# Optimization experiments

Hardware: AMD Instinct MI355X
Metric: run time of the kernel (lower is better)

The kernel has to match this reference:

```python
import jax, jax.numpy as jnp
import numpy as np

N, C_IN, C_OUT, K, S, P, H, W = 16, 64, 128, 3, 1, 1, 224, 224

def setup_inputs() -> dict:
    key = jax.random.key(0)
    kx, kw = jax.random.split(key)
    x = jax.random.normal(kx, (N, C_IN, H, W), dtype=jnp.float32)
    weight = jax.random.normal(kw, (C_OUT, C_IN, K, K), dtype=jnp.float32)
    bias = jnp.zeros((C_OUT,), dtype=jnp.float32)
    return {"x": x, "weight": weight, "bias": bias}

def reference(x, weight, bias):
    # im2col + matmul with stride 1 is exactly a standard conv2d with SAME-style padding P
    out = jax.lax.conv_general_dilated(
        x, weight,
        window_strides=(S, S),
        padding=((P, P), (P, P)),
        dimension_numbers=("NCHW", "OIHW", "NCHW"),
    )
    return out + bias[None, :, None, None]  # [N, C_OUT, H, W]
```

## Files before the change

### kernel.cpp

```cpp
#include <hip/hip_runtime.h>
#include <cstdint>
#include <cstddef>


typedef short bf16x8 __attribute__((ext_vector_type(8)));
typedef float f32x4 __attribute__((ext_vector_type(4)));

#define N_ 16
#define CI_ 64
#define CO_ 128
#define H_ 224
#define W_ 224
#define HW_ (H_ * W_)

#define WP_ 226
#define CBS_ 1808ULL
#define HPS_ 14464ULL
#define NS_ 3268864ULL

#define ROWBUF_SHORTS 7296
#define CONV3_LDS 145408

__device__ __forceinline__ unsigned short f2bf(float f) {
    unsigned u = __builtin_bit_cast(unsigned, f);
    u += 0x7FFFu + ((u >> 16) & 1u);
    return (unsigned short)(u >> 16);
}

__global__ void prep_weight(const float* __restrict__ w, unsigned short* __restrict__ wr) {
    int i = blockIdx.x * 256 + threadIdx.x;
    if (i >= 9 * CO_ * CI_) return;
    int ci = i & 63;
    int co = (i >> 6) & 127;
    int t  = i >> 13;
    wr[i] = f2bf(w[(co * CI_ + ci) * 9 + t]);
}

__global__ __launch_bounds__(256) void prep_x(const float* __restrict__ x,
                                              unsigned short* __restrict__ xp) {
    int b = blockIdx.x;
    int n = b / 226, hp = b - n * 226;
    int tid = threadIdx.x;
    unsigned short* row = xp + (size_t)n * NS_ + (size_t)hp * HPS_;
    if (hp == 0 || hp == 225) {
        #pragma unroll
        for (int k = 0; k < 8; ++k) {
            int i = k * 256 + tid;
            if (i < 1808) ((uint4*)row)[i] = make_uint4(0, 0, 0, 0);
        }
        return;
    }
    int h = hp - 1;
    const float* xb = x + (size_t)n * CI_ * HW_ + (size_t)h * W_;
    for (int k = 0; k < 7; ++k) {
        int item = k * 256 + tid;
        int w = item % 224;
        int cb = item / 224;
        unsigned r[4];
        #pragma unroll
        for (int c = 0; c < 4; ++c) {
            float lo = xb[(size_t)(cb * 8 + 2 * c) * HW_ + w];
            float hi = xb[(size_t)(cb * 8 + 2 * c + 1) * HW_ + w];
            r[c] = (unsigned)f2bf(lo) | ((unsigned)f2bf(hi) << 16);
        }
        *(uint4*)(row + (size_t)cb * CBS_ + (size_t)(w + 1) * 8) = make_uint4(r[0], r[1], r[2], r[3]);
    }
    if (tid < 16) {
        int cb = tid >> 1, wp = (tid & 1) * 225;
        *(uint4*)(row + (size_t)cb * CBS_ + (size_t)wp * 8) = make_uint4(0, 0, 0, 0);
    }
}

__global__ __launch_bounds__(512, 2) void conv3(
    const unsigned short* __restrict__ xp, const unsigned short* __restrict__ wr,
    const float* __restrict__ bias, float* __restrict__ out)
{
    extern __shared__ __align__(16) unsigned short ring[];
    float* bounce = (float*)ring + 6 * ROWBUF_SHORTS / 2;

    int bid = blockIdx.x;
    int swz = (bid & 7) * 32 + (bid >> 3);
    int n = swz >> 4;
    int rem = swz & 15;
    int wseg = rem & 1;
    int strip = rem >> 1;
    int ho0 = strip * 28;

    int tid = threadIdx.x, lane = tid & 63, wid = tid >> 6;
    int hr = wid & 1, mq = wid >> 1;
    int lrow = lane & 15, lk = lane >> 4;

    const unsigned short* xpn = xp + (size_t)n * NS_;

    auto stage_row = [&](int hp) {
        const unsigned short* srow = xpn + (size_t)hp * HPS_ + (size_t)(wseg * 112) * 8;
        unsigned short* dbase = ring + (size_t)(hp % 6) * ROWBUF_SHORTS;
        int idx = tid;
        {
            int cb = idx / 114, wp = idx - cb * 114;
            __builtin_amdgcn_global_load_lds(
                (const __attribute__((address_space(1))) void*)(srow + (size_t)cb * CBS_ + (size_t)wp * 8),
                (__attribute__((address_space(3))) void*)(dbase + (size_t)idx * 8), 16, 0, 0);
        }
        idx = 512 + tid;
        if (idx < 912) {
            int cb = idx / 114, wp = idx - cb * 114;
            __builtin_amdgcn_global_load_lds(
                (const __attribute__((address_space(1))) void*)(srow + (size_t)cb * CBS_ + (size_t)wp * 8),
                (__attribute__((address_space(3))) void*)(dbase + (size_t)idx * 8), 16, 0, 0);
        }
    };

    stage_row(ho0); stage_row(ho0 + 1); stage_row(ho0 + 2); stage_row(ho0 + 3);
    __syncthreads();

    #pragma unroll 1
    for (int i = 0; i < 14; ++i) {
        int ho = ho0 + 2 * i;

        if (i < 13) { stage_row(ho + 4); stage_row(ho + 5); }

        f32x4 acc[2][7];
        #pragma unroll
        for (int a = 0; a < 2; ++a)
            #pragma unroll
            for (int b2 = 0; b2 < 7; ++b2)
                #pragma unroll
                for (int k = 0; k < 4; ++k)
                    acc[a][b2][k] = 0.0f;

        #pragma unroll
        for (int ch = 0; ch < 2; ++ch) {
            #pragma unroll
            for (int t = 0; t < 9; ++t) {
                int kh = t / 3, kw = t - kh * 3;
                bf16x8 afr[2];
                #pragma unroll
                for (int mf = 0; mf < 2; ++mf) {
                    size_t ai = ((size_t)(t * 128 + mq * 32 + mf * 16 + lrow)) * 64
                              + (size_t)(ch * 32 + lk * 8);
                    afr[mf] = *(const bf16x8*)(wr + ai);
                }
                int slot = (ho + hr + kh) % 6;
                int rb = slot * ROWBUF_SHORTS + ((ch * 4 + lk) * 114) * 8;
                int wb = lrow + kw;
                #pragma unroll
                for (int nf = 0; nf < 7; ++nf) {
                    bf16x8 bfr = *(const bf16x8*)(ring + rb + (size_t)(wb + nf * 16) * 8);
                    acc[0][nf] = __builtin_amdgcn_mfma_f32_16x16x32_bf16(afr[0], bfr, acc[0][nf], 0, 0, 0);
                    acc[1][nf] = __builtin_amdgcn_mfma_f32_16x16x32_bf16(afr[1], bfr, acc[1][nf], 0, 0, 0);
                }
            }
        }

        float* lf = bounce + wid * 1808;
        int h = ho + hr;
        #pragma unroll
        for (int mf = 0; mf < 2; ++mf) {
            float bv[4];
            #pragma unroll
            for (int r = 0; r < 4; ++r)
                bv[r] = bias[mq * 32 + mf * 16 + lk * 4 + r];
            float* wbase = lf + lk * 452 + lrow;
            #pragma unroll
            for (int r = 0; r < 4; ++r)
                #pragma unroll
                for (int nf = 0; nf < 7; ++nf)
                    wbase[r * 112 + nf * 16] = acc[mf][nf][r] + bv[r];
            #pragma unroll
            for (int j = 0; j < 7; ++j) {
                int idx4 = j * 64 + lane;
                int col = idx4 / 28;
                int w4  = idx4 - col * 28;
                f32x4 v = *(const f32x4*)(lf + (col >> 2) * 452 + (col & 3) * 112 + w4 * 4);
                size_t ob = (((size_t)n * CO_ + mq * 32 + mf * 16 + col) * H_ + h) * W_
                          + wseg * 112 + w4 * 4;
                *(f32x4*)(out + ob) = v;
            }
        }

        __syncthreads();
    }
}

__global__ __launch_bounds__(256, 2) void conv2(
    const unsigned short* __restrict__ xp, const unsigned short* __restrict__ wr,
    const float* __restrict__ bias, float* __restrict__ out)
{
    __shared__ __align__(16) unsigned short xs[4 * 8 * 114 * 8];

    int bid = blockIdx.x;
    int swz = (bid & 7) * 448 + (bid >> 3);
    int n = swz / 224;
    int r2 = swz - n * 224;
    int hblk = r2 >> 1;
    int wseg = r2 & 1;
    int h0 = hblk * 2;

    int tid = threadIdx.x, lane = tid & 63, wid = tid >> 6;
    int hr = wid & 1, mh = wid >> 1;
    int lrow = lane & 15, lk = lane >> 4;

    f32x4 acc[4][7];
    #pragma unroll
    for (int a = 0; a < 4; ++a)
        #pragma unroll
        for (int b2 = 0; b2 < 7; ++b2)
            #pragma unroll
            for (int k = 0; k < 4; ++k)
                acc[a][b2][k] = 0.0f;

    const unsigned short* xpn = xp + (size_t)n * NS_;

    #pragma unroll
    for (int it = 0; it < 14; ++it) {
        int idx = it * 256 + tid;
        int wp = idx % 114;
        int rc = idx / 114;
        const unsigned short* src = xpn + (size_t)(h0 + (rc >> 3)) * HPS_
                                  + (size_t)(rc & 7) * CBS_ + (size_t)(wseg * 112 + wp) * 8;
        __builtin_amdgcn_global_load_lds(
            (const __attribute__((address_space(1))) void*)src,
            (__attribute__((address_space(3))) void*)(xs + (size_t)idx * 8), 16, 0, 0);
    }
    if (tid < 64) {
        int idx = 3584 + tid;
        int wp = idx % 114;
        int rc = idx / 114;
        const unsigned short* src = xpn + (size_t)(h0 + (rc >> 3)) * HPS_
                                  + (size_t)(rc & 7) * CBS_ + (size_t)(wseg * 112 + wp) * 8;
        __builtin_amdgcn_global_load_lds(
            (const __attribute__((address_space(1))) void*)src,
            (__attribute__((address_space(3))) void*)(xs + (size_t)idx * 8), 16, 0, 0);
    }
    __syncthreads();

    #pragma unroll
    for (int ch = 0; ch < 2; ++ch) {
        #pragma unroll
        for (int t = 0; t < 9; ++t) {
            int kh = t / 3, kw = t - kh * 3;
            bf16x8 afr[4];
            #pragma unroll
            for (int mf = 0; mf < 4; ++mf) {
                size_t ai = ((size_t)(t * 128 + mh * 64 + mf * 16 + lrow)) * 64
                          + (size_t)(ch * 32 + lk * 8);
                afr[mf] = *(const bf16x8*)(wr + ai);
            }
            int rbase = ((hr + kh) * 8 + ch * 4 + lk) * 114;
            int wpb = lrow + kw;
            #pragma unroll
            for (int nf = 0; nf < 7; ++nf) {
                bf16x8 bfr = *(const bf16x8*)(&xs[(size_t)(rbase + wpb + nf * 16) * 8]);
                #pragma unroll
                for (int mf = 0; mf < 4; ++mf)
                    acc[mf][nf] = __builtin_amdgcn_mfma_f32_16x16x32_bf16(
                        afr[mf], bfr, acc[mf][nf], 0, 0, 0);
            }
        }
    }

    __syncthreads();
    float* lf = (float*)xs;
    int h = h0 + hr;
    #pragma unroll
    for (int mf = 0; mf < 4; ++mf) {
        float bv[4];
        #pragma unroll
        for (int r = 0; r < 4; ++r)
            bv[r] = bias[mh * 64 + mf * 16 + lk * 4 + r];
        float* wbase = lf + wid * 1808 + lk * 452 + lrow;
        #pragma unroll
        for (int r = 0; r < 4; ++r)
            #pragma unroll
            for (int nf = 0; nf < 7; ++nf)
                wbase[r * 112 + nf * 16] = acc[mf][nf][r] + bv[r];
        #pragma unroll
        for (int j = 0; j < 7; ++j) {
            int idx4 = j * 64 + lane;
            int col = idx4 / 28;
            int w4  = idx4 - col * 28;
            f32x4 v = *(const f32x4*)(lf + wid * 1808 + (col >> 2) * 452 + (col & 3) * 112 + w4 * 4);
            size_t ob = (((size_t)n * CO_ + mh * 64 + mf * 16 + col) * H_ + h) * W_
                      + wseg * 112 + w4 * 4;
            *(f32x4*)(out + ob) = v;
        }
    }
}

__global__ __launch_bounds__(512, 2) void conv_mfma(
    const float* __restrict__ x, const unsigned short* __restrict__ wr,
    const float* __restrict__ bias, float* __restrict__ out)
{
    __shared__ unsigned short xs[4 * 4 * 226 * 8];
    int bid = blockIdx.x;
    int swz = (bid & 7) * 224 + (bid >> 3);
    int n = swz / 112;
    int hblk = swz - n * 112;
    int h0 = hblk * 2;
    int tid = threadIdx.x;
    int lane = tid & 63;
    int wid = tid >> 6;
    int hr = wid & 1, nh = (wid >> 1) & 1, mh = wid >> 2;
    int lrow = lane & 15, lk = lane >> 4;

    f32x4 acc[4][7];
    #pragma unroll
    for (int a = 0; a < 4; ++a)
        #pragma unroll
        for (int b = 0; b < 7; ++b)
            #pragma unroll
            for (int k = 0; k < 4; ++k)
                acc[a][b][k] = 0.0f;

    for (int ch = 0; ch < 2; ++ch) {
        if (ch) __syncthreads();
        const float* xb = x + ((size_t)n * CI_ + (size_t)ch * 32) * HW_;
        int wcol = tid % 224;
        int rem = tid / 224;
        for (int it = 0; it < 7; ++it) {
            float v[8]; int bi[8];
            #pragma unroll
            for (int u = 0; u < 8; ++u) {
                int ciL = rem & 31;
                int r4 = rem >> 5;
                int hh = h0 - 1 + r4;
                float val = 0.0f;
                if ((unsigned)hh < (unsigned)H_)
                    val = xb[(size_t)ciL * HW_ + (size_t)hh * W_ + wcol];
                v[u] = val;
                bi[u] = (((r4 << 2) + (ciL >> 3)) * 226 + wcol + 1) * 8 + (ciL & 7);
                wcol += 64; rem += 2;
                if (wcol >= 224) { wcol -= 224; rem += 1; }
            }
            #pragma unroll
            for (int u = 0; u < 8; ++u)
                xs[bi[u]] = f2bf(v[u]);
        }
        if (tid < 256) {
            int wp = (tid & 1) * 225;
            int ciL = (tid >> 1) & 31;
            int r4 = tid >> 6;
            xs[(((r4 << 2) + (ciL >> 3)) * 226 + wp) * 8 + (ciL & 7)] = 0;
        }
        __syncthreads();

        #pragma unroll
        for (int t = 0; t < 9; ++t) {
            int kh = t / 3, kw = t - kh * 3;
            bf16x8 afr[4];
            #pragma unroll
            for (int mf = 0; mf < 4; ++mf) {
                size_t ai = ((size_t)(t * 128 + mh * 64 + mf * 16 + lrow)) * 64
                          + (size_t)(ch * 32 + lk * 8);
                afr[mf] = *(const bf16x8*)(wr + ai);
            }
            int rbase = ((hr + kh) * 4 + lk) * 226;
            int wpb = nh * 112 + lrow + kw;
            #pragma unroll
            for (int nf = 0; nf < 7; ++nf) {
                bf16x8 bfr = *(const bf16x8*)(&xs[(size_t)(rbase + wpb + nf * 16) * 8]);
                #pragma unroll
                for (int mf = 0; mf < 4; ++mf)
                    acc[mf][nf] = __builtin_amdgcn_mfma_f32_16x16x32_bf16(
                        afr[mf], bfr, acc[mf][nf], 0, 0, 0);
            }
        }
    }

    int h = h0 + hr;
    #pragma unroll
    for (int mf = 0; mf < 4; ++mf) {
        #pragma unroll
        for (int r = 0; r < 4; ++r) {
            int co = mh * 64 + mf * 16 + lk * 4 + r;
            float bv = bias[co];
            size_t ob = (((size_t)n * CO_ + co) * H_ + h) * W_ + nh * 112 + lrow;
            #pragma unroll
            for (int nf = 0; nf < 7; ++nf)
                out[ob + (size_t)nf * 16] = acc[mf][nf][r] + bv;
        }
    }
}

extern "C" void kernel_launch(void* const* d_in, const int* in_sizes, int n_in,
                              void* d_out, int out_size, void* d_ws, size_t ws_size,
                              hipStream_t stream) {
    const float* x    = (const float*)d_in[0];
    const float* w    = (const float*)d_in[1];
    const float* bias = (const float*)d_in[2];
    float* out = (float*)d_out;
    unsigned short* wr = (unsigned short*)d_ws;
    const size_t xp_bytes = (size_t)N_ * NS_ * 2;
    const size_t need = 147456 + xp_bytes;

    prep_weight<<<dim3(288), dim3(256), 0, stream>>>(w, wr);
    if (ws_size >= need) {
        unsigned short* xp = wr + 73728;
        prep_x<<<dim3(16 * 226), dim3(256), 0, stream>>>(x, xp);
        hipError_t e = hipFuncSetAttribute(
            reinterpret_cast<const void*>(conv3),
            hipFuncAttributeMaxDynamicSharedMemorySize, CONV3_LDS);
        if (e == hipSuccess) {
            conv3<<<dim3(256), dim3(512), CONV3_LDS, stream>>>(xp, wr, bias, out);
        } else {
            conv2<<<dim3(16 * 112 * 2), dim3(256), 0, stream>>>(xp, wr, bias, out);
        }
    } else {
        conv_mfma<<<dim3(16 * 112), dim3(512), 0, stream>>>(x, wr, bias, out);
    }
}
```

Before: 243.8 us.

## Fuse input bf16 conversion into conv kernel with register-staged prefetch

Removes the separate prep_x pass that wrote a padded bf16 copy of x to workspace. The conv3 kernel now reads fp32 x directly, converts it to bf16 and writes it into its LDS ring buffer. Loads for the next two rows are issued into registers before the MFMA loop and stored to LDS after it, to overlap global latency with compute. Bias loads are hoisted out of the loop. This saves a full write and re-read of the converted input but replaces async global_load_lds with strided per-channel fp32 scalar loads, and it raises register pressure through the 32-float prefetch buffer.

```diff
diff --git a/kernel.cpp b/kernel.cpp
--- a/kernel.cpp
+++ b/kernel.cpp
@@ -36,43 +36,8 @@
     wr[i] = f2bf(w[(co * CI_ + ci) * 9 + t]);
 }
 
-__global__ __launch_bounds__(256) void prep_x(const float* __restrict__ x,
-                                              unsigned short* __restrict__ xp) {
-    int b = blockIdx.x;
-    int n = b / 226, hp = b - n * 226;
-    int tid = threadIdx.x;
-    unsigned short* row = xp + (size_t)n * NS_ + (size_t)hp * HPS_;
-    if (hp == 0 || hp == 225) {
-        #pragma unroll
-        for (int k = 0; k < 8; ++k) {
-            int i = k * 256 + tid;
-            if (i < 1808) ((uint4*)row)[i] = make_uint4(0, 0, 0, 0);
-        }
-        return;
-    }
-    int h = hp - 1;
-    const float* xb = x + (size_t)n * CI_ * HW_ + (size_t)h * W_;
-    for (int k = 0; k < 7; ++k) {
-        int item = k * 256 + tid;
-        int w = item % 224;
-        int cb = item / 224;
-        unsigned r[4];
-        #pragma unroll
-        for (int c = 0; c < 4; ++c) {
-            float lo = xb[(size_t)(cb * 8 + 2 * c) * HW_ + w];
-            float hi = xb[(size_t)(cb * 8 + 2 * c + 1) * HW_ + w];
-            r[c] = (unsigned)f2bf(lo) | ((unsigned)f2bf(hi) << 16);
-        }
-        *(uint4*)(row + (size_t)cb * CBS_ + (size_t)(w + 1) * 8) = make_uint4(r[0], r[1], r[2], r[3]);
-    }
-    if (tid < 16) {
-        int cb = tid >> 1, wp = (tid & 1) * 225;
-        *(uint4*)(row + (size_t)cb * CBS_ + (size_t)wp * 8) = make_uint4(0, 0, 0, 0);
-    }
-}
-
 __global__ __launch_bounds__(512, 2) void conv3(
-    const unsigned short* __restrict__ xp, const unsigned short* __restrict__ wr,
+    const float* __restrict__ x, const unsigned short* __restrict__ wr,
     const float* __restrict__ bias, float* __restrict__ out)
 {
     extern __shared__ __align__(16) unsigned short ring[];
@@ -90,35 +55,61 @@
     int hr = wid & 1, mq = wid >> 1;
     int lrow = lane & 15, lk = lane >> 4;
 
-    const unsigned short* xpn = xp + (size_t)n * NS_;
-
-    auto stage_row = [&](int hp) {
-        const unsigned short* srow = xpn + (size_t)hp * HPS_ + (size_t)(wseg * 112) * 8;
-        unsigned short* dbase = ring + (size_t)(hp % 6) * ROWBUF_SHORTS;
-        int idx = tid;
-        {
-            int cb = idx / 114, wp = idx - cb * 114;
-            __builtin_amdgcn_global_load_lds(
-                (const __attribute__((address_space(1))) void*)(srow + (size_t)cb * CBS_ + (size_t)wp * 8),
-                (__attribute__((address_space(3))) void*)(dbase + (size_t)idx * 8), 16, 0, 0);
-        }
-        idx = 512 + tid;
-        if (idx < 912) {
-            int cb = idx / 114, wp = idx - cb * 114;
-            __builtin_amdgcn_global_load_lds(
-                (const __attribute__((address_space(1))) void*)(srow + (size_t)cb * CBS_ + (size_t)wp * 8),
-                (__attribute__((address_space(3))) void*)(dbase + (size_t)idx * 8), 16, 0, 0);
-        }
-    };
-
-    stage_row(ho0); stage_row(ho0 + 1); stage_row(ho0 + 2); stage_row(ho0 + 3);
+    const float* xn = x + (size_t)n * CI_ * HW_;
+
+    float bv[2][4];
+    #pragma unroll
+    for (int mf = 0; mf < 2; ++mf)
+        #pragma unroll
+        for (int r = 0; r < 4; ++r)
+            bv[mf][r] = bias[mq * 32 + mf * 16 + lk * 4 + r];
+
+    #pragma unroll
+    for (int r8 = 0; r8 < 8; ++r8) {
+        int idx = r8 * 512 + tid;
+        if (idx < 3648) {
+            int row = idx / 912;
+            int rc  = idx - row * 912;
+            int cb  = rc / 114, wp = rc - cb * 114;
+            int hp  = ho0 + row;
+            int h   = hp - 1;
+            int w   = wseg * 112 + wp - 1;
+            bool ok = ((unsigned)h < (unsigned)H_) & ((unsigned)w < (unsigned)W_);
+            const float* src = xn + ((size_t)cb * 8) * HW_ + (size_t)h * W_ + w;
+            float v[8];
+            #pragma unroll
+            for (int c = 0; c < 8; ++c)
+                v[c] = ok ? src[(size_t)c * HW_] : 0.0f;
+            unsigned d[4];
+            #pragma unroll
+            for (int c = 0; c < 4; ++c)
+                d[c] = (unsigned)f2bf(v[2 * c]) | ((unsigned)f2bf(v[2 * c + 1]) << 16);
+            *(uint4*)(ring + (size_t)(hp % 6) * ROWBUF_SHORTS + (size_t)rc * 8)
+                = make_uint4(d[0], d[1], d[2], d[3]);
+        }
+    }
     __syncthreads();
 
     #pragma unroll 1
     for (int i = 0; i < 14; ++i) {
         int ho = ho0 + 2 * i;
 
-        if (i < 13) { stage_row(ho + 4); stage_row(ho + 5); }
+        float pv[4][8];
+        #pragma unroll
+        for (int k = 0; k < 4; ++k) {
+            int idx = k * 512 + tid;
+            bool act = (i < 13) && (idx < 1824);
+            int row = idx / 912;
+            int rc  = idx - row * 912;
+            int cb  = rc / 114, wp = rc - cb * 114;
+            int h   = ho + 3 + row;
+            int w   = wseg * 112 + wp - 1;
+            bool ok = act & ((unsigned)h < (unsigned)H_) & ((unsigned)w < (unsigned)W_);
+            const float* src = xn + ((size_t)cb * 8) * HW_ + (size_t)h * W_ + w;
+            #pragma unroll
+            for (int c = 0; c < 8; ++c)
+                pv[k][c] = ok ? src[(size_t)c * HW_] : 0.0f;
+        }
 
         f32x4 acc[2][7];
         #pragma unroll
@@ -153,20 +144,34 @@
             }
         }
 
+        if (i < 13) {
+            #pragma unroll
+            for (int k = 0; k < 4; ++k) {
+                int idx = k * 512 + tid;
+                if (idx < 1824) {
+                    int row = idx / 912;
+                    int rc  = idx - row * 912;
+                    int hp  = ho + 4 + row;
+                    unsigned d[4];
+                    #pragma unroll
+                    for (int c = 0; c < 4; ++c)
+                        d[c] = (unsigned)f2bf(pv[k][2 * c]) | ((unsigned)f2bf(pv[k][2 * c + 1]) << 16);
+                    *(uint4*)(ring + (size_t)(hp % 6) * ROWBUF_SHORTS + (size_t)rc * 8)
+                        = make_uint4(d[0], d[1], d[2], d[3]);
+                }
+            }
+        }
+
         float* lf = bounce + wid * 1808;
         int h = ho + hr;
         #pragma unroll
         for (int mf = 0; mf < 2; ++mf) {
-            float bv[4];
+            float* wbase = lf + lk * 452 + lrow;
             #pragma unroll
             for (int r = 0; r < 4; ++r)
-                bv[r] = bias[mq * 32 + mf * 16 + lk * 4 + r];
-            float* wbase = lf + lk * 452 + lrow;
-            #pragma unroll
-            for (int r = 0; r < 4; ++r)
                 #pragma unroll
                 for (int nf = 0; nf < 7; ++nf)
-                    wbase[r * 112 + nf * 16] = acc[mf][nf][r] + bv[r];
+                    wbase[r * 112 + nf * 16] = acc[mf][nf][r] + bv[mf][r];
             #pragma unroll
             for (int j = 0; j < 7; ++j) {
                 int idx4 = j * 64 + lane;
@@ -180,6 +185,41 @@
         }
 
         __syncthreads();
+    }
+}
+
+__global__ __launch_bounds__(256) void prep_x(const float* __restrict__ x,
+                                              unsigned short* __restrict__ xp) {
+    int b = blockIdx.x;
+    int n = b / 226, hp = b - n * 226;
+    int tid = threadIdx.x;
+    unsigned short* row = xp + (size_t)n * NS_ + (size_t)hp * HPS_;
+    if (hp == 0 || hp == 225) {
+        #pragma unroll
+        for (int k = 0; k < 8; ++k) {
+            int i = k * 256 + tid;
+            if (i < 1808) ((uint4*)row)[i] = make_uint4(0, 0, 0, 0);
+        }
+        return;
+    }
+    int h = hp - 1;
+    const float* xb = x + (size_t)n * CI_ * HW_ + (size_t)h * W_;
+    for (int k = 0; k < 7; ++k) {
+        int item = k * 256 + tid;
+        int w = item % 224;
+        int cb = item / 224;
+        unsigned r[4];
+        #pragma unroll
+        for (int c = 0; c < 4; ++c) {
+            float lo = xb[(size_t)(cb * 8 + 2 * c) * HW_ + w];
+            float hi = xb[(size_t)(cb * 8 + 2 * c + 1) * HW_ + w];
+            r[c] = (unsigned)f2bf(lo) | ((unsigned)f2bf(hi) << 16);
+        }
+        *(uint4*)(row + (size_t)cb * CBS_ + (size_t)(w + 1) * 8) = make_uint4(r[0], r[1], r[2], r[3]);
+    }
+    if (tid < 16) {
+        int cb = tid >> 1, wp = (tid & 1) * 225;
+        *(uint4*)(row + (size_t)cb * CBS_ + (size_t)wp * 8) = make_uint4(0, 0, 0, 0);
     }
 }
 
@@ -288,101 +328,6 @@
     }
 }
 
-__global__ __launch_bounds__(512, 2) void conv_mfma(
-    const float* __restrict__ x, const unsigned short* __restrict__ wr,
-    const float* __restrict__ bias, float* __restrict__ out)
-{
-    __shared__ unsigned short xs[4 * 4 * 226 * 8];
-    int bid = blockIdx.x;
-    int swz = (bid & 7) * 224 + (bid >> 3);
-    int n = swz / 112;
-    int hblk = swz - n * 112;
-    int h0 = hblk * 2;
-    int tid = threadIdx.x;
-    int lane = tid & 63;
-    int wid = tid >> 6;
-    int hr = wid & 1, nh = (wid >> 1) & 1, mh = wid >> 2;
-    int lrow = lane & 15, lk = lane >> 4;
-
-    f32x4 acc[4][7];
-    #pragma unroll
-    for (int a = 0; a < 4; ++a)
-        #pragma unroll
-        for (int b = 0; b < 7; ++b)
-            #pragma unroll
-            for (int k = 0; k < 4; ++k)
-                acc[a][b][k] = 0.0f;
-
-    for (int ch = 0; ch < 2; ++ch) {
-        if (ch) __syncthreads();
-        const float* xb = x + ((size_t)n * CI_ + (size_t)ch * 32) * HW_;
-        int wcol = tid % 224;
-        int rem = tid / 224;
-        for (int it = 0; it < 7; ++it) {
-            float v[8]; int bi[8];
-            #pragma unroll
-            for (int u = 0; u < 8; ++u) {
-                int ciL = rem & 31;
-                int r4 = rem >> 5;
-                int hh = h0 - 1 + r4;
-                float val = 0.0f;
-                if ((unsigned)hh < (unsigned)H_)
-                    val = xb[(size_t)ciL * HW_ + (size_t)hh * W_ + wcol];
-                v[u] = val;
-                bi[u] = (((r4 << 2) + (ciL >> 3)) * 226 + wcol + 1) * 8 + (ciL & 7);
-                wcol += 64; rem += 2;
-                if (wcol >= 224) { wcol -= 224; rem += 1; }
-            }
-            #pragma unroll
-            for (int u = 0; u < 8; ++u)
-                xs[bi[u]] = f2bf(v[u]);
-        }
-        if (tid < 256) {
-            int wp = (tid & 1) * 225;
-            int ciL = (tid >> 1) & 31;
-            int r4 = tid >> 6;
-            xs[(((r4 << 2) + (ciL >> 3)) * 226 + wp) * 8 + (ciL & 7)] = 0;
-        }
-        __syncthreads();
-
-        #pragma unroll
-        for (int t = 0; t < 9; ++t) {
-            int kh = t / 3, kw = t - kh * 3;
-            bf16x8 afr[4];
-            #pragma unroll
-            for (int mf = 0; mf < 4; ++mf) {
-                size_t ai = ((size_t)(t * 128 + mh * 64 + mf * 16 + lrow)) * 64
-                          + (size_t)(ch * 32 + lk * 8);
-                afr[mf] = *(const bf16x8*)(wr + ai);
-            }
-            int rbase = ((hr + kh) * 4 + lk) * 226;
-            int wpb = nh * 112 + lrow + kw;
-            #pragma unroll
-            for (int nf = 0; nf < 7; ++nf) {
-                bf16x8 bfr = *(const bf16x8*)(&xs[(size_t)(rbase + wpb + nf * 16) * 8]);
-                #pragma unroll
-                for (int mf = 0; mf < 4; ++mf)
-                    acc[mf][nf] = __builtin_amdgcn_mfma_f32_16x16x32_bf16(
-                        afr[mf], bfr, acc[mf][nf], 0, 0, 0);
-            }
-        }
-    }
-
-    int h = h0 + hr;
-    #pragma unroll
-    for (int mf = 0; mf < 4; ++mf) {
-        #pragma unroll
-        for (int r = 0; r < 4; ++r) {
-            int co = mh * 64 + mf * 16 + lk * 4 + r;
-            float bv = bias[co];
-            size_t ob = (((size_t)n * CO_ + co) * H_ + h) * W_ + nh * 112 + lrow;
-            #pragma unroll
-            for (int nf = 0; nf < 7; ++nf)
-                out[ob + (size_t)nf * 16] = acc[mf][nf][r] + bv;
-        }
-    }
-}
-
 extern "C" void kernel_launch(void* const* d_in, const int* in_sizes, int n_in,
                               void* d_out, int out_size, void* d_ws, size_t ws_size,
                               hipStream_t stream) {
@@ -391,22 +336,20 @@
     const float* bias = (const float*)d_in[2];
     float* out = (float*)d_out;
     unsigned short* wr = (unsigned short*)d_ws;
-    const size_t xp_bytes = (size_t)N_ * NS_ * 2;
-    const size_t need = 147456 + xp_bytes;
 
     prep_weight<<<dim3(288), dim3(256), 0, stream>>>(w, wr);
-    if (ws_size >= need) {
-        unsigned short* xp = wr + 73728;
-        prep_x<<<dim3(16 * 226), dim3(256), 0, stream>>>(x, xp);
-        hipError_t e = hipFuncSetAttribute(
-            reinterpret_cast<const void*>(conv3),
-            hipFuncAttributeMaxDynamicSharedMemorySize, CONV3_LDS);
-        if (e == hipSuccess) {
-            conv3<<<dim3(256), dim3(512), CONV3_LDS, stream>>>(xp, wr, bias, out);
-        } else {
+
+    hipError_t e = hipFuncSetAttribute(
+        reinterpret_cast<const void*>(conv3),
+        hipFuncAttributeMaxDynamicSharedMemorySize, CONV3_LDS);
+    if (e == hipSuccess) {
+        conv3<<<dim3(256), dim3(512), CONV3_LDS, stream>>>(x, wr, bias, out);
+    } else {
+        const size_t xp_bytes = (size_t)N_ * NS_ * 2;
+        if (ws_size >= 147456 + xp_bytes) {
+            unsigned short* xp = wr + 73728;
+            prep_x<<<dim3(16 * 226), dim3(256), 0, stream>>>(x, xp);
             conv2<<<dim3(16 * 112 * 2), dim3(256), 0, stream>>>(xp, wr, bias, out);
         }
-    } else {
-        conv_mfma<<<dim3(16 * 112), dim3(512), 0, stream>>>(x, wr, bias, out);
-    }
-}
+    }
+}
```

After: 438.1 us. 79.7% more time.
